# Performance work log

Hardware: AMD Instinct MI355X
Metric: run time of the kernel (lower is better)

The kernel has to match this reference:

```python
import jax, jax.numpy as jnp
import numpy as np

D_MODEL = 512
N_HEADS = 8
D_HEAD = D_MODEL // N_HEADS


def setup_inputs() -> dict:
    key = jax.random.key(0)
    ks = jax.random.split(key, 11)
    B, S = 2, 4096
    scale = 1.0 / np.sqrt(D_MODEL)
    inp = {
        "q": jax.random.normal(ks[0], (B, S, D_MODEL), dtype=jnp.float32),
        "k": jax.random.normal(ks[1], (B, S, D_MODEL), dtype=jnp.float32),
        "v": jax.random.normal(ks[2], (B, S, D_MODEL), dtype=jnp.float32),
        "Wq": jax.random.normal(ks[3], (D_MODEL, D_MODEL), dtype=jnp.float32) * scale,
        "bq": jnp.zeros((D_MODEL,), dtype=jnp.float32),
        "Wk": jax.random.normal(ks[4], (D_MODEL, D_MODEL), dtype=jnp.float32) * scale,
        "bk": jnp.zeros((D_MODEL,), dtype=jnp.float32),
        "Wv": jax.random.normal(ks[5], (D_MODEL, D_MODEL), dtype=jnp.float32) * scale,
        "bv": jnpp if False else jnp.zeros((D_MODEL,), dtype=jnp.float32),
        "Wo": jax.random.normal(ks[6], (D_MODEL, D_MODEL), dtype=jnp.float32) * scale,
        "bo": jnp.zeros((D_MODEL,), dtype=jnp.float32),
    }
    return inp


def reference(q, k, v, Wq, bq, Wk, bk, Wv, bv, Wo, bo):
    B, S, _ = q.shape
    # Linear projections (torch Linear: x @ W^T + b), split into heads -> [B,H,S,Dh]
    def proj(x, W, b):
        y = jnp.einsum("bsd,ed->bse", x, W) + b
        return y.reshape(B, -1, N_HEADS, D_HEAD).transpose(0, 2, 1, 3)

    Q = proj(q, Wq, bq)
    K = proj(k, Wk, bk)
    V = proj(v, Wv, bv)

    inv_sqrt_dh = 1.0 / np.sqrt(D_HEAD).astype(np.float32)
    scores = jnp.einsum("bhqd,bhkd->bhqk", Q, K) * inv_sqrt_dh  # [B,H,S,S]
    attn = jax.nn.softmax(scores, axis=-1)  # dropout is identity at eval
    out = jnp.einsum("bhqk,bhkd->bhqd", attn, V)  # [B,H,S,Dh]
    out = out.transpose(0, 2, 1, 3).reshape(B, S, D_MODEL)
    return jnp.einsum("bsd,ed->bse", out, Wo) + bo
```

## Files before the change

kernel.cpp:

```cpp
#include <hip/hip_runtime.h>
#include <hip/hip_bf16.h>
#include <hip/hip_fp16.h>
#include <stdint.h>

#define D_MODEL 512
#define NH 8
#define DH 64
#define BB 2
#define SS 4096
#define MTOT (BB*SS)

typedef __attribute__((ext_vector_type(8))) short bf16x8;
typedef __attribute__((ext_vector_type(4))) short bf16x4;
typedef __attribute__((ext_vector_type(4))) float f32x4;
typedef __fp16 fp16x2 __attribute__((ext_vector_type(2)));

#define MFMA32(a,b,c) __builtin_amdgcn_mfma_f32_16x16x32_bf16(a,b,c,0,0,0)

#if __has_builtin(__builtin_amdgcn_exp2f)
  #define EXP2F(x) __builtin_amdgcn_exp2f(x)
#else
  #define EXP2F(x) __expf((x) * 0.6931471805599453f)
#endif

#define QSCALE 0.18033688011112042f
#define EXPOFF 11.541560327679939f

__device__ __forceinline__ unsigned f2b(float f) {
  return (__float_as_uint(f) + 0x8000u) >> 16;
}
__device__ __forceinline__ float h2f(unsigned short h) {
  return __half2float(__ushort_as_half(h));
}
__device__ __forceinline__ unsigned packh2(float lo, float hi) {
  fp16x2 h = __builtin_amdgcn_cvt_pkrtz(lo, hi);
  return __builtin_bit_cast(unsigned, h);
}
__device__ __forceinline__ unsigned packpair(float lo, float hi) {
  return __builtin_amdgcn_perm(__float_as_uint(hi) + 0x8000u,
                               __float_as_uint(lo) + 0x8000u, 0x07060302u);
}
__device__ __forceinline__ unsigned cvtpk_bf16(float lo, float hi) {
  unsigned r;
  asm("v_cvt_pk_bf16_f32 %0, %1, %2" : "=v"(r) : "v"(lo), "v"(hi));
  return r;
}

struct PrepArgs {
  const float* src[7];
  unsigned short* dst[7];
  int off[8];
};

__global__ __launch_bounds__(256) void prep_kernel(PrepArgs a) {
  const int bx = blockIdx.x;
  int tgt = 0;
#pragma unroll
  for (int s = 1; s < 7; s++) tgt += (bx >= a.off[s]);
  const int i = ((bx - a.off[tgt]) * 256 + threadIdx.x) * 4;
  const float4 f = *(const float4*)(a.src[tgt] + i);
  uint2 o;
  o.x = packpair(f.x, f.y);
  o.y = packpair(f.z, f.w);
  *(uint2*)(a.dst[tgt] + i) = o;
}

struct CombArgs {
  const unsigned short* Os[4];
  const float* ls[4];
  unsigned short* Ao;
};

__global__ __launch_bounds__(256) void combine_kernel(CombArgs c) {
  const size_t i = ((size_t)blockIdx.x * 256 + threadIdx.x) * 8;
  const int m = (int)(i >> 9);
  const int k = (int)(i & 511);
  const int hh = k >> 6;
  const float inv = __builtin_amdgcn_rcpf(
      c.ls[0][(size_t)m * NH + hh] + c.ls[1][(size_t)m * NH + hh] +
      c.ls[2][(size_t)m * NH + hh] + c.ls[3][(size_t)m * NH + hh]);
  float sum[8] = {0.f, 0.f, 0.f, 0.f, 0.f, 0.f, 0.f, 0.f};
#pragma unroll
  for (int s = 0; s < 4; s++) {
    uint4 hv = *(const uint4*)(c.Os[s] + i);
    const unsigned short* he = (const unsigned short*)&hv;
#pragma unroll
    for (int e = 0; e < 8; e++) sum[e] += h2f(he[e]);
  }
  uint4 pk;
  pk.x = packpair(sum[0] * inv, sum[1] * inv);
  pk.y = packpair(sum[2] * inv, sum[3] * inv);
  pk.z = packpair(sum[4] * inv, sum[5] * inv);
  pk.w = packpair(sum[6] * inv, sum[7] * inv);
  *(uint4*)(c.Ao + i) = pk;
}

struct GemmArgs {
  const unsigned short* A[3];
  const unsigned short* W[3];
  const float* bias[3];
  unsigned short* out[3];
  float* outf;
  int mode;
};

__global__ __launch_bounds__(256) void gemm_kernel(GemmArgs g) {
  const int z = blockIdx.z;
  const float* __restrict__ bias = g.bias[z];
  unsigned short* __restrict__ out = g.out[z];
  const bool vt = (g.mode == 0) && (z == 2);
  const float osc = (g.mode == 0 && z == 0) ? QSCALE : 1.0f;

  __shared__ __align__(16) unsigned short lA[128][40];
  __shared__ __align__(16) unsigned short lB[128][40];

  const int t = threadIdx.x;
  const int lane = t & 63;
  const int w = t >> 6;
  const int wr = w >> 1, wc = w & 1;
  const int lrow = lane & 15, quad = lane >> 4;
  const int m0 = blockIdx.y * 128;
  const int n0 = blockIdx.x * 128;

  f32x4 acc[4][4];
  for (int i = 0; i < 4; i++)
    for (int j = 0; j < 4; j++)
      for (int r = 0; r < 4; r++) acc[i][j][r] = 0.f;

  for (int kk = 0; kk < 512; kk += 32) {
#pragma unroll
    for (int i = 0; i < 2; i++) {
      int id = t + i * 256;
      int row = id >> 2;
      int c8 = (id & 3) * 8;
      *(uint4*)&lA[row][c8] = *(const uint4*)(g.A[z] + (size_t)(m0 + row) * 512 + kk + c8);
      *(uint4*)&lB[row][c8] = *(const uint4*)(g.W[z] + (size_t)(n0 + row) * 512 + kk + c8);
    }
    __syncthreads();
    bf16x8 af[4], bfr[4];
#pragma unroll
    for (int mt = 0; mt < 4; mt++) af[mt] = *(const bf16x8*)&lA[wr * 64 + mt * 16 + lrow][quad * 8];
#pragma unroll
    for (int nt = 0; nt < 4; nt++) bfr[nt] = *(const bf16x8*)&lB[wc * 64 + nt * 16 + lrow][quad * 8];
#pragma unroll
    for (int mt = 0; mt < 4; mt++)
#pragma unroll
      for (int nt = 0; nt < 4; nt++)
        acc[mt][nt] = MFMA32(af[mt], bfr[nt], acc[mt][nt]);
    __syncthreads();
  }

  float bv[4];
#pragma unroll
  for (int nt = 0; nt < 4; nt++) bv[nt] = bias[n0 + wc * 64 + nt * 16 + lrow];

#pragma unroll
  for (int mt = 0; mt < 4; mt++) {
#pragma unroll
    for (int nt = 0; nt < 4; nt++) {
      const int n = n0 + wc * 64 + nt * 16 + lrow;
      const int mB = m0 + wr * 64 + mt * 16 + quad * 4;
      float val[4];
#pragma unroll
      for (int r = 0; r < 4; r++) val[r] = (acc[mt][nt][r] + bv[nt]) * osc;

      if (g.mode == 1) {
#pragma unroll
        for (int r = 0; r < 4; r++) g.outf[(size_t)(mB + r) * 512 + n] = val[r];
      } else if (vt) {
        const int bb = mB >> 12, s = mB & 4095;
        const int a = s >> 2;
        const int c0 = (s & ~31) + (a & 4) + ((a & 3) << 3);
        const int hh = n >> 6, dh = n & 63;
        ushort4 pk = make_ushort4((unsigned short)f2b(val[0]), (unsigned short)f2b(val[1]),
                                  (unsigned short)f2b(val[2]), (unsigned short)f2b(val[3]));
        *(ushort4*)(out + (((size_t)bb * NH + hh) * DH + dh) * SS + c0) = pk;
      } else {
        const int bb = mB >> 12;
        const int hh = n >> 6, dh = n & 63;
#pragma unroll
        for (int r = 0; r < 4; r++) {
          const int s = (mB + r) & 4095;
          out[((((size_t)bb * NH + hh) * SS + s) << 6) + dh] = (unsigned short)f2b(val[r]);
        }
      }
    }
  }
}

struct AttnArgs {
  const unsigned short* Qh;
  const unsigned short* Kh;
  const unsigned short* Vt;
  unsigned short* Op[4];
  float* lp[4];
};

__global__ __launch_bounds__(512, 4) void attn_kernel(AttnArgs a) {
  __shared__ __align__(16) unsigned short lK[64][72];
  __shared__ __align__(16) unsigned short lV[64][72];

  const int t = threadIdx.x;
  const int lane = t & 63;
  const int w = t >> 6;
  const int lrow = lane & 15, quad = lane >> 4;
  const int h = blockIdx.y, b = blockIdx.z;
  const int qtile = blockIdx.x & 15, jq = blockIdx.x >> 4;
  const size_t kb = ((size_t)b * NH + h) * SS * DH;
  const size_t vb = ((size_t)b * NH + h) * DH * SS;
  const int qrow0 = qtile * 256 + w * 32;
  unsigned short* __restrict__ Op = a.Op[jq];
  float* __restrict__ lp = a.lp[jq];
  const int jt0 = jq * 16, jt1 = jt0 + 16;

  bf16x8 qf[2][2];
#pragma unroll
  for (int ti = 0; ti < 2; ti++) {
    const unsigned short* qp = a.Qh + kb + (size_t)(qrow0 + ti * 16 + lrow) * DH + quad * 8;
    qf[ti][0] = *(const bf16x8*)qp;
    qf[ti][1] = *(const bf16x8*)(qp + 32);
  }

  f32x4 o[2][4];
  float lsum[2] = {0.f, 0.f};
#pragma unroll
  for (int ti = 0; ti < 2; ti++)
    for (int nt = 0; nt < 4; nt++)
      for (int r = 0; r < 4; r++) o[ti][nt][r] = 0.f;

  const unsigned short* __restrict__ Kg = a.Kh + kb;
  const unsigned short* __restrict__ Vg = a.Vt + vb;

  const int rk = t >> 3;
  const int ck = (t & 7) * 8;

  uint4 kreg = *(const uint4*)(Kg + (size_t)(jt0 * 64 + rk) * DH + ck);
  uint4 vreg = *(const uint4*)(Vg + (size_t)rk * SS + jt0 * 64 + ck);

  const f32x4 sinit = {-EXPOFF, -EXPOFF, -EXPOFF, -EXPOFF};

  for (int jt = jt0; jt < jt1; jt++) {
    __syncthreads();
    *(uint4*)&lK[rk][ck] = kreg;
    *(uint4*)&lV[rk][ck] = vreg;
    {
      const int nb = (jt + 1 < jt1 ? jt + 1 : jt) * 64;
      kreg = *(const uint4*)(Kg + (size_t)(nb + rk) * DH + ck);
      vreg = *(const uint4*)(Vg + (size_t)rk * SS + nb + ck);
    }
    __syncthreads();

#pragma unroll
    for (int half = 0; half < 2; half++) {
      uint2 pw[2][2];
#pragma unroll
      for (int u = 0; u < 2; u++) {
        const int ntj = half * 2 + u;
        bf16x8 k0 = *(const bf16x8*)&lK[ntj * 16 + lrow][quad * 8];
        bf16x8 k1 = *(const bf16x8*)&lK[ntj * 16 + lrow][32 + quad * 8];
#pragma unroll
        for (int ti = 0; ti < 2; ti++) {
          f32x4 s = MFMA32(k0, qf[ti][0], sinit);
          s = MFMA32(k1, qf[ti][1], s);
          const float e0 = EXP2F(s[0]);
          const float e1 = EXP2F(s[1]);
          const float e2 = EXP2F(s[2]);
          const float e3 = EXP2F(s[3]);
          lsum[ti] += (e0 + e1) + (e2 + e3);
          pw[u][ti].x = cvtpk_bf16(e0, e1);
          pw[u][ti].y = cvtpk_bf16(e2, e3);
        }
      }
      bf16x8 pcat[2];
#pragma unroll
      for (int ti = 0; ti < 2; ti++) {
        uint4 c;
        c.x = pw[0][ti].x; c.y = pw[0][ti].y;
        c.z = pw[1][ti].x; c.w = pw[1][ti].y;
        pcat[ti] = __builtin_bit_cast(bf16x8, c);
      }
#pragma unroll
      for (int nt = 0; nt < 4; nt++) {
        bf16x8 vv = *(const bf16x8*)&lV[nt * 16 + lrow][half * 32 + quad * 8];
#pragma unroll
        for (int ti = 0; ti < 2; ti++)
          o[ti][nt] = MFMA32(vv, pcat[ti], o[ti][nt]);
      }
    }
  }

#pragma unroll
  for (int ti = 0; ti < 2; ti++) {
    float l = lsum[ti];
    l += __shfl_xor(l, 16);
    l += __shfl_xor(l, 32);
    const int si = qrow0 + ti * 16 + lrow;
    unsigned short* dst = Op + ((size_t)(b * SS + si)) * D_MODEL + h * DH;
#pragma unroll
    for (int nt = 0; nt < 4; nt++) {
      uint2 pk;
      pk.x = packh2(o[ti][nt][0], o[ti][nt][1]);
      pk.y = packh2(o[ti][nt][2], o[ti][nt][3]);
      *(uint2*)(dst + nt * 16 + quad * 4) = pk;
    }
    if (quad == 0)
      lp[(size_t)(b * SS + si) * NH + h] = l;
  }
}

extern "C" void kernel_launch(void* const* d_in, const int* in_sizes, int n_in,
                              void* d_out, int out_size, void* d_ws, size_t ws_size,
                              hipStream_t stream) {
  const float* q  = (const float*)d_in[0];
  const float* k  = (const float*)d_in[1];
  const float* v  = (const float*)d_in[2];
  const float* Wq = (const float*)d_in[3];
  const float* bq = (const float*)d_in[4];
  const float* Wk = (const float*)d_in[5];
  const float* bk = (const float*)d_in[6];
  const float* Wv = (const float*)d_in[7];
  const float* bv = (const float*)d_in[8];
  const float* Wo = (const float*)d_in[9];
  const float* bo = (const float*)d_in[10];

  const size_t NX = (size_t)MTOT * D_MODEL;
  const size_t NW = (size_t)D_MODEL * D_MODEL;

  char* p = (char*)d_ws;
  unsigned short* qb  = (unsigned short*)p; p += NX * 2;
  unsigned short* kbf = (unsigned short*)p; p += NX * 2;
  unsigned short* vbf = (unsigned short*)p; p += NX * 2;
  unsigned short* Wqb = (unsigned short*)p; p += NW * 2;
  unsigned short* Wkb = (unsigned short*)p; p += NW * 2;
  unsigned short* Wvb = (unsigned short*)p; p += NW * 2;
  unsigned short* Wob = (unsigned short*)p; p += NW * 2;
  unsigned short* Qh  = (unsigned short*)p; p += NX * 2;
  unsigned short* Kh  = (unsigned short*)p; p += NX * 2;
  unsigned short* Vtg = (unsigned short*)p; p += NX * 2;
  unsigned short* Ao  = (unsigned short*)p; p += NX * 2;
  unsigned short* Os[4];
  float* ls[4];
  for (int i = 0; i < 4; i++) { Os[i] = (unsigned short*)p; p += NX * 2; }
  for (int i = 0; i < 4; i++) { ls[i] = (float*)p; p += (size_t)MTOT * NH * 4; }

  PrepArgs pr;
  pr.src[0] = q;  pr.dst[0] = qb;
  pr.src[1] = k;  pr.dst[1] = kbf;
  pr.src[2] = v;  pr.dst[2] = vbf;
  pr.src[3] = Wq; pr.dst[3] = Wqb;
  pr.src[4] = Wk; pr.dst[4] = Wkb;
  pr.src[5] = Wv; pr.dst[5] = Wvb;
  pr.src[6] = Wo; pr.dst[6] = Wob;
  {
    const int nb[7] = {(int)(NX / 1024), (int)(NX / 1024), (int)(NX / 1024),
                       (int)(NW / 1024), (int)(NW / 1024), (int)(NW / 1024),
                       (int)(NW / 1024)};
    int acc = 0;
    for (int i = 0; i < 7; i++) { pr.off[i] = acc; acc += nb[i]; }
    pr.off[7] = acc;
    prep_kernel<<<dim3(acc, 1, 1), 256, 0, stream>>>(pr);
  }

  GemmArgs pa;
  pa.A[0] = qb; pa.A[1] = kbf; pa.A[2] = vbf;
  pa.W[0] = Wqb; pa.W[1] = Wkb; pa.W[2] = Wvb;
  pa.bias[0] = bq; pa.bias[1] = bk; pa.bias[2] = bv;
  pa.out[0] = Qh; pa.out[1] = Kh; pa.out[2] = Vtg;
  pa.outf = nullptr;
  pa.mode = 0;
  gemm_kernel<<<dim3(4, 64, 3), 256, 0, stream>>>(pa);

  AttnArgs aa;
  aa.Qh = Qh; aa.Kh = Kh; aa.Vt = Vtg;
  for (int i = 0; i < 4; i++) { aa.Op[i] = Os[i]; aa.lp[i] = ls[i]; }
  attn_kernel<<<dim3(64, NH, BB), 512, 0, stream>>>(aa);

  CombArgs ca;
  for (int i = 0; i < 4; i++) { ca.Os[i] = Os[i]; ca.ls[i] = ls[i]; }
  ca.Ao = Ao;
  combine_kernel<<<dim3((int)(NX / 8 / 256), 1, 1), 256, 0, stream>>>(ca);

  GemmArgs oa;
  oa.A[0] = Ao; oa.A[1] = Ao; oa.A[2] = Ao;
  oa.W[0] = Wob; oa.W[1] = Wob; oa.W[2] = Wob;
  oa.bias[0] = bo; oa.bias[1] = bo; oa.bias[2] = bo;
  oa.out[0] = nullptr; oa.out[1] = nullptr; oa.out[2] = nullptr;
  oa.outf = (float*)d_out;
  oa.mode = 1;
  gemm_kernel<<<dim3(4, 64, 1), 256, 0, stream>>>(oa);
}
```

Measured before the change: 235.9 us.

## Fuse fp32-to-bf16 conversion and split-KV combine into GEMM loads; prioritize MFMA

Drops the separate prep kernel: the projection GEMM now reads fp32 inputs and weights and converts to bf16 while staging tiles in LDS. The combine kernel is replaced by a tiny reciprocal-normalizer kernel, and the output GEMM sums the four fp16 partial outputs and scales them on the fly while loading its A tile. Setprio hints are wrapped around the MFMA blocks in attention. This removes two kernel launches and intermediate bf16 buffer round-trips, at the cost of doubled global read bytes in the GEMM loads and the partial-sum combine being redone for each of the four column-tile blocks.

Measured after the change: 249.5 us. 1.06x slower.

```diff
diff --git a/kernel.cpp b/kernel.cpp
--- a/kernel.cpp
+++ b/kernel.cpp
@@ -11,7 +11,6 @@
 #define MTOT (BB*SS)
 
 typedef __attribute__((ext_vector_type(8))) short bf16x8;
-typedef __attribute__((ext_vector_type(4))) short bf16x4;
 typedef __attribute__((ext_vector_type(4))) float f32x4;
 typedef __fp16 fp16x2 __attribute__((ext_vector_type(2)));
 
@@ -45,62 +44,44 @@
   asm("v_cvt_pk_bf16_f32 %0, %1, %2" : "=v"(r) : "v"(lo), "v"(hi));
   return r;
 }
-
-struct PrepArgs {
-  const float* src[7];
-  unsigned short* dst[7];
-  int off[8];
+__device__ __forceinline__ uint4 ld8_f32_to_bf16(const float* p) {
+  const float4 a0 = *(const float4*)p;
+  const float4 a1 = *(const float4*)(p + 4);
+  uint4 v;
+  v.x = packpair(a0.x, a0.y);
+  v.y = packpair(a0.z, a0.w);
+  v.z = packpair(a1.x, a1.y);
+  v.w = packpair(a1.z, a1.w);
+  return v;
+}
+
+struct LinvArgs {
+  const float* ls[4];
+  float* linv;
 };
 
-__global__ __launch_bounds__(256) void prep_kernel(PrepArgs a) {
-  const int bx = blockIdx.x;
-  int tgt = 0;
-#pragma unroll
-  for (int s = 1; s < 7; s++) tgt += (bx >= a.off[s]);
-  const int i = ((bx - a.off[tgt]) * 256 + threadIdx.x) * 4;
-  const float4 f = *(const float4*)(a.src[tgt] + i);
-  uint2 o;
-  o.x = packpair(f.x, f.y);
-  o.y = packpair(f.z, f.w);
-  *(uint2*)(a.dst[tgt] + i) = o;
-}
-
-struct CombArgs {
-  const unsigned short* Os[4];
-  const float* ls[4];
-  unsigned short* Ao;
-};
-
-__global__ __launch_bounds__(256) void combine_kernel(CombArgs c) {
-  const size_t i = ((size_t)blockIdx.x * 256 + threadIdx.x) * 8;
-  const int m = (int)(i >> 9);
-  const int k = (int)(i & 511);
-  const int hh = k >> 6;
-  const float inv = __builtin_amdgcn_rcpf(
-      c.ls[0][(size_t)m * NH + hh] + c.ls[1][(size_t)m * NH + hh] +
-      c.ls[2][(size_t)m * NH + hh] + c.ls[3][(size_t)m * NH + hh]);
-  float sum[8] = {0.f, 0.f, 0.f, 0.f, 0.f, 0.f, 0.f, 0.f};
-#pragma unroll
-  for (int s = 0; s < 4; s++) {
-    uint4 hv = *(const uint4*)(c.Os[s] + i);
-    const unsigned short* he = (const unsigned short*)&hv;
-#pragma unroll
-    for (int e = 0; e < 8; e++) sum[e] += h2f(he[e]);
-  }
-  uint4 pk;
-  pk.x = packpair(sum[0] * inv, sum[1] * inv);
-  pk.y = packpair(sum[2] * inv, sum[3] * inv);
-  pk.z = packpair(sum[4] * inv, sum[5] * inv);
-  pk.w = packpair(sum[6] * inv, sum[7] * inv);
-  *(uint4*)(c.Ao + i) = pk;
+__global__ __launch_bounds__(256) void linv_kernel(LinvArgs la) {
+  const int i = (blockIdx.x * 256 + threadIdx.x) * 4;
+  const float4 a = *(const float4*)(la.ls[0] + i);
+  const float4 b = *(const float4*)(la.ls[1] + i);
+  const float4 c = *(const float4*)(la.ls[2] + i);
+  const float4 d = *(const float4*)(la.ls[3] + i);
+  float4 o;
+  o.x = __builtin_amdgcn_rcpf(a.x + b.x + c.x + d.x);
+  o.y = __builtin_amdgcn_rcpf(a.y + b.y + c.y + d.y);
+  o.z = __builtin_amdgcn_rcpf(a.z + b.z + c.z + d.z);
+  o.w = __builtin_amdgcn_rcpf(a.w + b.w + c.w + d.w);
+  *(float4*)(la.linv + i) = o;
 }
 
 struct GemmArgs {
-  const unsigned short* A[3];
-  const unsigned short* W[3];
+  const float* Af[3];
+  const float* Wf[3];
   const float* bias[3];
   unsigned short* out[3];
   float* outf;
+  const unsigned short* Os[4];
+  const float* linv;
   int mode;
 };
 
@@ -128,13 +109,39 @@
       for (int r = 0; r < 4; r++) acc[i][j][r] = 0.f;
 
   for (int kk = 0; kk < 512; kk += 32) {
-#pragma unroll
-    for (int i = 0; i < 2; i++) {
-      int id = t + i * 256;
-      int row = id >> 2;
-      int c8 = (id & 3) * 8;
-      *(uint4*)&lA[row][c8] = *(const uint4*)(g.A[z] + (size_t)(m0 + row) * 512 + kk + c8);
-      *(uint4*)&lB[row][c8] = *(const uint4*)(g.W[z] + (size_t)(n0 + row) * 512 + kk + c8);
+    if (g.mode == 0) {
+#pragma unroll
+      for (int i = 0; i < 2; i++) {
+        const int id = t + i * 256;
+        const int row = id >> 2;
+        const int c8 = (id & 3) * 8;
+        *(uint4*)&lA[row][c8] = ld8_f32_to_bf16(g.Af[z] + (size_t)(m0 + row) * 512 + kk + c8);
+        *(uint4*)&lB[row][c8] = ld8_f32_to_bf16(g.Wf[z] + (size_t)(n0 + row) * 512 + kk + c8);
+      }
+    } else {
+#pragma unroll
+      for (int i = 0; i < 2; i++) {
+        const int id = t + i * 256;
+        const int row = id >> 2;
+        const int c8 = (id & 3) * 8;
+        const size_t off = (size_t)(m0 + row) * 512 + kk + c8;
+        float s[8] = {0.f, 0.f, 0.f, 0.f, 0.f, 0.f, 0.f, 0.f};
+#pragma unroll
+        for (int sl = 0; sl < 4; sl++) {
+          const uint4 hv = *(const uint4*)(g.Os[sl] + off);
+          const unsigned short* he = (const unsigned short*)&hv;
+#pragma unroll
+          for (int e = 0; e < 8; e++) s[e] += h2f(he[e]);
+        }
+        const float inv = g.linv[(size_t)(m0 + row) * NH + ((kk + c8) >> 6)];
+        uint4 av;
+        av.x = packpair(s[0] * inv, s[1] * inv);
+        av.y = packpair(s[2] * inv, s[3] * inv);
+        av.z = packpair(s[4] * inv, s[5] * inv);
+        av.w = packpair(s[6] * inv, s[7] * inv);
+        *(uint4*)&lA[row][c8] = av;
+        *(uint4*)&lB[row][c8] = ld8_f32_to_bf16(g.Wf[0] + (size_t)(n0 + row) * 512 + kk + c8);
+      }
     }
     __syncthreads();
     bf16x8 af[4], bfr[4];
@@ -260,8 +267,10 @@
         bf16x8 k1 = *(const bf16x8*)&lK[ntj * 16 + lrow][32 + quad * 8];
 #pragma unroll
         for (int ti = 0; ti < 2; ti++) {
+          __builtin_amdgcn_s_setprio(1);
           f32x4 s = MFMA32(k0, qf[ti][0], sinit);
           s = MFMA32(k1, qf[ti][1], s);
+          __builtin_amdgcn_s_setprio(0);
           const float e0 = EXP2F(s[0]);
           const float e1 = EXP2F(s[1]);
           const float e2 = EXP2F(s[2]);
@@ -279,6 +288,7 @@
         c.z = pw[1][ti].x; c.w = pw[1][ti].y;
         pcat[ti] = __builtin_bit_cast(bf16x8, c);
       }
+      __builtin_amdgcn_s_setprio(1);
 #pragma unroll
       for (int nt = 0; nt < 4; nt++) {
         bf16x8 vv = *(const bf16x8*)&lV[nt * 16 + lrow][half * 32 + quad * 8];
@@ -286,6 +296,7 @@
         for (int ti = 0; ti < 2; ti++)
           o[ti][nt] = MFMA32(vv, pcat[ti], o[ti][nt]);
       }
+      __builtin_amdgcn_s_setprio(0);
     }
   }
 
@@ -324,49 +335,25 @@
   const float* bo = (const float*)d_in[10];
 
   const size_t NX = (size_t)MTOT * D_MODEL;
-  const size_t NW = (size_t)D_MODEL * D_MODEL;
 
   char* p = (char*)d_ws;
-  unsigned short* qb  = (unsigned short*)p; p += NX * 2;
-  unsigned short* kbf = (unsigned short*)p; p += NX * 2;
-  unsigned short* vbf = (unsigned short*)p; p += NX * 2;
-  unsigned short* Wqb = (unsigned short*)p; p += NW * 2;
-  unsigned short* Wkb = (unsigned short*)p; p += NW * 2;
-  unsigned short* Wvb = (unsigned short*)p; p += NW * 2;
-  unsigned short* Wob = (unsigned short*)p; p += NW * 2;
   unsigned short* Qh  = (unsigned short*)p; p += NX * 2;
   unsigned short* Kh  = (unsigned short*)p; p += NX * 2;
   unsigned short* Vtg = (unsigned short*)p; p += NX * 2;
-  unsigned short* Ao  = (unsigned short*)p; p += NX * 2;
   unsigned short* Os[4];
   float* ls[4];
   for (int i = 0; i < 4; i++) { Os[i] = (unsigned short*)p; p += NX * 2; }
   for (int i = 0; i < 4; i++) { ls[i] = (float*)p; p += (size_t)MTOT * NH * 4; }
-
-  PrepArgs pr;
-  pr.src[0] = q;  pr.dst[0] = qb;
-  pr.src[1] = k;  pr.dst[1] = kbf;
-  pr.src[2] = v;  pr.dst[2] = vbf;
-  pr.src[3] = Wq; pr.dst[3] = Wqb;
-  pr.src[4] = Wk; pr.dst[4] = Wkb;
-  pr.src[5] = Wv; pr.dst[5] = Wvb;
-  pr.src[6] = Wo; pr.dst[6] = Wob;
-  {
-    const int nb[7] = {(int)(NX / 1024), (int)(NX / 1024), (int)(NX / 1024),
-                       (int)(NW / 1024), (int)(NW / 1024), (int)(NW / 1024),
-                       (int)(NW / 1024)};
-    int acc = 0;
-    for (int i = 0; i < 7; i++) { pr.off[i] = acc; acc += nb[i]; }
-    pr.off[7] = acc;
-    prep_kernel<<<dim3(acc, 1, 1), 256, 0, stream>>>(pr);
-  }
+  float* linv = (float*)p; p += (size_t)MTOT * NH * 4;
 
   GemmArgs pa;
-  pa.A[0] = qb; pa.A[1] = kbf; pa.A[2] = vbf;
-  pa.W[0] = Wqb; pa.W[1] = Wkb; pa.W[2] = Wvb;
+  pa.Af[0] = q;  pa.Af[1] = k;  pa.Af[2] = v;
+  pa.Wf[0] = Wq; pa.Wf[1] = Wk; pa.Wf[2] = Wv;
   pa.bias[0] = bq; pa.bias[1] = bk; pa.bias[2] = bv;
   pa.out[0] = Qh; pa.out[1] = Kh; pa.out[2] = Vtg;
   pa.outf = nullptr;
+  for (int i = 0; i < 4; i++) pa.Os[i] = nullptr;
+  pa.linv = nullptr;
   pa.mode = 0;
   gemm_kernel<<<dim3(4, 64, 3), 256, 0, stream>>>(pa);
 
@@ -375,17 +362,19 @@
   for (int i = 0; i < 4; i++) { aa.Op[i] = Os[i]; aa.lp[i] = ls[i]; }
   attn_kernel<<<dim3(64, NH, BB), 512, 0, stream>>>(aa);
 
-  CombArgs ca;
-  for (int i = 0; i < 4; i++) { ca.Os[i] = Os[i]; ca.ls[i] = ls[i]; }
-  ca.Ao = Ao;
-  combine_kernel<<<dim3((int)(NX / 8 / 256), 1, 1), 256, 0, stream>>>(ca);
+  LinvArgs la;
+  for (int i = 0; i < 4; i++) la.ls[i] = ls[i];
+  la.linv = linv;
+  linv_kernel<<<dim3((int)(MTOT * NH / 4 / 256), 1, 1), 256, 0, stream>>>(la);
 
   GemmArgs oa;
-  oa.A[0] = Ao; oa.A[1] = Ao; oa.A[2] = Ao;
-  oa.W[0] = Wob; oa.W[1] = Wob; oa.W[2] = Wob;
-  oa.bias[0] = bo; oa.bias[1] = bo; oa.bias[2] = bo;
+  oa.Af[0] = nullptr; oa.Af[1] = nullptr; oa.Af[2] = nullptr;
+  oa.Wf[0] = Wo; oa.Wf[1] = nullptr; oa.Wf[2] = nullptr;
+  oa.bias[0] = bo; oa.bias[1] = nullptr; oa.bias[2] = nullptr;
   oa.out[0] = nullptr; oa.out[1] = nullptr; oa.out[2] = nullptr;
   oa.outf = (float*)d_out;
+  for (int i = 0; i < 4; i++) oa.Os[i] = Os[i];
+  oa.linv = linv;
   oa.mode = 1;
   gemm_kernel<<<dim3(4, 64, 1), 256, 0, stream>>>(oa);
 }
```
